# Performance work log

Hardware: AMD Instinct MI355X
Metric: run time of the kernel (lower is better)

Reference implementation:

```python
import jax, jax.numpy as jnp
import numpy as np

NUM_HEADS = 16
KERNEL_SIZE = 13


def setup_inputs() -> dict:
    key = jax.random.key(0)
    ks = jax.random.split(key, 6)
    B, L, C = 4, 4096, 512
    H, K = NUM_HEADS, KERNEL_SIZE
    x = jax.random.normal(ks[0], (B, L, C), dtype=jnp.float32)
    qkv_w = jax.random.normal(ks[1], (C, 3 * C), dtype=jnp.float32) * 0.02
    qkv_b = jnp.zeros((3 * C,), dtype=jnp.float32)
    rpb = jax.random.normal(ks[2], (H, 2 * K - 1), dtype=jnp.float32) * 0.02
    proj_w = jax.random.normal(ks[3], (C, C), dtype=jnp.float32) * 0.02
    proj_b = jnp.zeros((C,), dtype=jnp.float32)
    return {"x": x, "qkv_w": qkv_w, "qkv_b": qkv_b, "rpb": rpb,
            "proj_w": proj_w, "proj_b": proj_b}


def reference(x, qkv_w, qkv_b, rpb, proj_w, proj_b):
    B, L, C = x.shape
    H, K = NUM_HEADS, KERNEL_SIZE
    hd = C // H
    scale = hd ** -0.5
    kh = K // 2

    # qkv projection -> q,k,v each [B,H,L,hd]
    qkv = (x @ qkv_w + qkv_b).reshape(B, L, 3, H, hd).transpose(2, 0, 3, 1, 4)
    q, k, v = qkv[0] * scale, qkv[1], qkv[2]

    # NATTEN window: start index clamped so window stays in-bounds
    pos = jnp.arange(L)
    ni = jnp.clip(pos - kh, 0, L - K)              # [L] window start per query
    idx = ni[:, None] + jnp.arange(K)[None, :]     # [L,K] key positions
    # rpb index: (key_pos - query_pos) + (K-1)
    rpb_idx = (ni - pos + (K - 1))[:, None] + jnp.arange(K)[None, :]  # [L,K]

    k_win = k[:, :, idx, :]                        # [B,H,L,K,hd]
    v_win = v[:, :, idx, :]                        # [B,H,L,K,hd]

    attn = jnp.einsum('bhld,bhlkd->bhlk', q, k_win) + rpb[:, rpb_idx][None]
    attn = jax.nn.softmax(attn, axis=-1)

    out = jnp.einsum('bhlk,bhlkd->bhld', attn, v_win)  # [B,H,L,hd]
    out = out.transpose(0, 2, 1, 3).reshape(B, L, C)
    return out @ proj_w + proj_b
```

## Files before the change

kernel.cpp:

```cpp
#include <hip/hip_runtime.h>
#include <hip/hip_bf16.h>
#include <stdint.h>


typedef __attribute__((ext_vector_type(8))) short short8;
typedef __attribute__((ext_vector_type(4))) float f32x4;
typedef __attribute__((ext_vector_type(8))) unsigned short u16x8;
typedef __attribute__((ext_vector_type(4))) float float4v;

#define NB 4
#define NL 4096
#define NC 512
#define NH 16
#define HD 32
#define KW 13
#define KHALF 6
#define NM (NB*NL)

__device__ __forceinline__ float b2f(unsigned short u) {
  union { unsigned int i; float f; } x; x.i = ((unsigned int)u) << 16; return x.f;
}
__device__ __forceinline__ unsigned short f2b(float f) {
  __hip_bfloat16 h = __float2bfloat16(f);
  return __builtin_bit_cast(unsigned short, h);
}
__device__ __forceinline__ void gll16(const unsigned short* g, unsigned short* l) {
  __builtin_amdgcn_global_load_lds(
      (const __attribute__((address_space(1))) void*)g,
      (__attribute__((address_space(3))) void*)l, 16, 0, 0);
}

__global__ __launch_bounds__(256) void cvt_f32_bf16(const float* __restrict__ in,
                                                    unsigned short* __restrict__ out) {
  long i = (long)blockIdx.x * 256 + threadIdx.x;
  const float4v* in4 = (const float4v*)in;
  float4v a = in4[i * 2];
  float4v b = in4[i * 2 + 1];
  u16x8 u;
  u[0] = f2b(a.x); u[1] = f2b(a.y); u[2] = f2b(a.z); u[3] = f2b(a.w);
  u[4] = f2b(b.x); u[5] = f2b(b.y); u[6] = f2b(b.z); u[7] = f2b(b.w);
  ((u16x8*)out)[i] = u;
}

__global__ __launch_bounds__(256) void transpose_bf16(const float* __restrict__ in,
                                                      unsigned short* __restrict__ out,
                                                      int R, int C) {
  __shared__ float t[32][33];
  int c0 = blockIdx.x * 32;
  int r0 = blockIdx.y * 32;
  int tx = threadIdx.x;
  int ty = threadIdx.y;
  #pragma unroll
  for (int i = ty; i < 32; i += 8)
    t[i][tx] = in[(long)(r0 + i) * C + c0 + tx];
  __syncthreads();
  #pragma unroll
  for (int i = ty; i < 32; i += 8)
    out[(long)(c0 + i) * R + r0 + tx] = f2b(t[tx][i]);
}


__device__ __forceinline__ void stage_half(const unsigned short* __restrict__ G,
                                           long rowBase, int K, int kt,
                                           unsigned short* ldsDst, int tid) {
  int r  = tid >> 3;
  int ch = (tid & 7) ^ (r & 7);
  const unsigned short* s0 = G + (rowBase + r) * (long)K + kt * 64 + ch * 8;
  gll16(s0, ldsDst + tid * 8);
  gll16(s0 + 64 * (long)K, ldsDst + 4096 + tid * 8);
}

#define BAR() __builtin_amdgcn_s_barrier()
#define LGK0() asm volatile("s_waitcnt lgkmcnt(0)" ::: "memory")
#define VM(N) asm volatile("s_waitcnt vmcnt(" #N ")" ::: "memory")

#define DS_A(BUF, QM) do { \
  const char* _ba = (const char*)(lds + (BUF)*16384 + wm*8192); \
  _Pragma("unroll") for (int ii = 0; ii < 4; ++ii) { \
    int _row = ((QM)*4+ii)*16 + lr; \
    _Pragma("unroll") for (int kb = 0; kb < 2; ++kb) \
      af[ii][kb] = *(const short8*)(_ba + _row*128 + (((kb*4+lk) ^ lr7) * 16)); \
  } \
} while (0)

#define DS_B(BUF, QN, BF) do { \
  const char* _bb = (const char*)(lds + 32768 + (BUF)*16384 + (wn>>1)*8192); \
  _Pragma("unroll") for (int jj = 0; jj < 2; ++jj) { \
    int _row = (wn&1)*64 + ((QN)*2+jj)*16 + lr; \
    _Pragma("unroll") for (int kb = 0; kb < 2; ++kb) \
      BF[jj][kb] = *(const short8*)(_bb + _row*128 + (((kb*4+lk) ^ lr7) * 16)); \
  } \
} while (0)

#define MMA(QM, QN, BF) do { \
  __builtin_amdgcn_s_setprio(1); \
  _Pragma("unroll") for (int ii = 0; ii < 4; ++ii) \
    _Pragma("unroll") for (int jj = 0; jj < 2; ++jj) \
      _Pragma("unroll") for (int kb = 0; kb < 2; ++kb) \
        acc[(QM)*4+ii][(QN)*2+jj] = __builtin_amdgcn_mfma_f32_16x16x32_bf16( \
            af[ii][kb], BF[jj][kb], acc[(QM)*4+ii][(QN)*2+jj], 0, 0, 0); \
  __builtin_amdgcn_s_setprio(0); \
} while (0)

template<int OUT_BF16>
__global__ __launch_bounds__(512, 2)
void gemm256(const unsigned short* __restrict__ A,
             const unsigned short* __restrict__ BT,
             const float* __restrict__ bias,
             void* __restrict__ Cout,
             int M, int N, int K, int tilesN) {
  __shared__ __align__(16) unsigned short lds[65536];

  int tid = threadIdx.x;
  int nwg = gridDim.x;
  int cpx = nwg >> 3;
  int wg  = ((int)blockIdx.x & 7) * cpx + ((int)blockIdx.x >> 3);
  int tm = wg / tilesN, tn = wg % tilesN;
  long mBase = (long)tm * 256;
  long nBase = (long)tn * 256;

  int lane = tid & 63, wave = tid >> 6;
  int wm = wave >> 2;
  int wn = wave & 3;
  int lr = lane & 15, lk = lane >> 4, lr7 = lr & 7;

  unsigned short* A0h0 = lds;
  unsigned short* A0h1 = lds + 8192;
  unsigned short* A1h0 = lds + 16384;
  unsigned short* A1h1 = lds + 16384 + 8192;
  unsigned short* B0h0 = lds + 32768;
  unsigned short* B0h1 = lds + 32768 + 8192;
  unsigned short* B1h0 = lds + 32768 + 16384;
  unsigned short* B1h1 = lds + 32768 + 16384 + 8192;

  f32x4 acc[8][4];
  #pragma unroll
  for (int i = 0; i < 8; ++i)
    #pragma unroll
    for (int j = 0; j < 4; ++j) acc[i][j] = (f32x4){0.f, 0.f, 0.f, 0.f};

  short8 af[4][2], bf0[2][2], bf1[2][2];

  stage_half(BT, nBase,       K, 0, B0h0, tid);
  stage_half(BT, nBase + 128, K, 0, B0h1, tid);
  stage_half(A,  mBase,       K, 0, A0h0, tid);
  stage_half(A,  mBase + 128, K, 0, A0h1, tid);
  stage_half(BT, nBase,       K, 1, B1h0, tid);
  stage_half(BT, nBase + 128, K, 1, B1h1, tid);
  VM(4);
  BAR();

  #pragma unroll 1
  for (int it = 0; it < 4; ++it) {
    int kt = it * 2;
    bool s2 = (kt + 2) < 8;
    bool s3 = (kt + 3) < 8;

    DS_A(0, 0);
    DS_B(0, 0, bf0);
    stage_half(A, mBase, K, kt + 1, A1h0, tid);
    BAR(); LGK0();
    MMA(0, 0, bf0);
    BAR();
    DS_B(0, 1, bf1);
    stage_half(A, mBase + 128, K, kt + 1, A1h1, tid);
    BAR(); LGK0();
    MMA(0, 1, bf1);
    BAR();
    DS_A(0, 1);
    if (s2) stage_half(BT, nBase, K, kt + 2, B0h0, tid);
    BAR(); LGK0();
    MMA(1, 1, bf1);
    BAR();
    if (s2) { stage_half(BT, nBase + 128, K, kt + 2, B0h1, tid); VM(4); }
    else    { VM(0); }
    BAR();
    MMA(1, 0, bf0);
    BAR();
    DS_A(1, 0);
    DS_B(1, 0, bf0);
    if (s2) stage_half(A, mBase, K, kt + 2, A0h0, tid);
    BAR(); LGK0();
    MMA(0, 0, bf0);
    BAR();
    DS_B(1, 1, bf1);
    if (s2) stage_half(A, mBase + 128, K, kt + 2, A0h1, tid);
    BAR(); LGK0();
    MMA(0, 1, bf1);
    BAR();
    DS_A(1, 1);
    if (s3) stage_half(BT, nBase, K, kt + 3, B1h0, tid);
    BAR(); LGK0();
    MMA(1, 1, bf1);
    BAR();
    if (s3) { stage_half(BT, nBase + 128, K, kt + 3, B1h1, tid); VM(4); }
    BAR();
    MMA(1, 0, bf0);
    BAR();
  }

  long rowb = mBase + wm * 128 + (lane >> 4) * 4;
  int  colb = (int)nBase + wn * 64 + lr;
  if (OUT_BF16) {
    unsigned short* C = (unsigned short*)Cout;
    #pragma unroll
    for (int mi = 0; mi < 8; ++mi)
      #pragma unroll
      for (int nj = 0; nj < 4; ++nj) {
        int col = colb + nj * 16;
        float bv = bias[col];
        #pragma unroll
        for (int r = 0; r < 4; ++r)
          C[(rowb + mi * 16 + r) * (long)N + col] = f2b(acc[mi][nj][r] + bv);
      }
  } else {
    float* C = (float*)Cout;
    #pragma unroll
    for (int mi = 0; mi < 8; ++mi)
      #pragma unroll
      for (int nj = 0; nj < 4; ++nj) {
        int col = colb + nj * 16;
        float bv = bias[col];
        #pragma unroll
        for (int r = 0; r < 4; ++r)
          C[(rowb + mi * 16 + r) * (long)N + col] = acc[mi][nj][r] + bv;
      }
  }
}

__global__ __launch_bounds__(256)
void natt(const unsigned short* __restrict__ qkv, const float* __restrict__ rpb,
          unsigned short* __restrict__ out) {
  int tid = blockIdx.x * 256 + threadIdx.x;
  int h = tid & 15;
  int l = (tid >> 4) & (NL - 1);
  int b = tid >> 16;
  const float scale = 0.17677669529663687f;

  long qb = ((long)(b * NL + l) * 3) * NC + h * HD;
  float q[HD];
  {
    const u16x8* q8 = (const u16x8*)(qkv + qb);
    #pragma unroll
    for (int w = 0; w < 4; ++w) {
      u16x8 u = q8[w];
      #pragma unroll
      for (int e = 0; e < 8; ++e) q[w * 8 + e] = b2f(u[e]) * scale;
    }
  }

  int ni = l - KHALF;
  if (ni < 0) ni = 0;
  if (ni > NL - KW) ni = NL - KW;
  const float* rb = rpb + h * (2 * KW - 1) + (ni - l + KW - 1);

  float p[KW];
  float mx = -1e30f;
  #pragma unroll
  for (int j = 0; j < KW; ++j) {
    long kb = ((long)(b * NL + ni + j) * 3 + 1) * NC + h * HD;
    const u16x8* k8 = (const u16x8*)(qkv + kb);
    float s = 0.f;
    #pragma unroll
    for (int w = 0; w < 4; ++w) {
      u16x8 u = k8[w];
      #pragma unroll
      for (int e = 0; e < 8; ++e) s += q[w * 8 + e] * b2f(u[e]);
    }
    s += rb[j];
    p[j] = s;
    mx = fmaxf(mx, s);
  }

  float sum = 0.f;
  #pragma unroll
  for (int j = 0; j < KW; ++j) { p[j] = __expf(p[j] - mx); sum += p[j]; }
  float inv = 1.0f / sum;

  float o[HD];
  #pragma unroll
  for (int d = 0; d < HD; ++d) o[d] = 0.f;
  #pragma unroll
  for (int j = 0; j < KW; ++j) {
    long vb = ((long)(b * NL + ni + j) * 3 + 2) * NC + h * HD;
    const u16x8* v8 = (const u16x8*)(qkv + vb);
    float wj = p[j] * inv;
    #pragma unroll
    for (int w = 0; w < 4; ++w) {
      u16x8 u = v8[w];
      #pragma unroll
      for (int e = 0; e < 8; ++e) o[w * 8 + e] += wj * b2f(u[e]);
    }
  }

  unsigned short* op = out + (long)(b * NL + l) * NC + h * HD;
  #pragma unroll
  for (int w = 0; w < 4; ++w) {
    u16x8 u;
    #pragma unroll
    for (int e = 0; e < 8; ++e) u[e] = f2b(o[w * 8 + e]);
    *((u16x8*)(op + w * 8)) = u;
  }
}

extern "C" void kernel_launch(void* const* d_in, const int* in_sizes, int n_in,
                              void* d_out, int out_size, void* d_ws, size_t ws_size,
                              hipStream_t stream) {
  const float* x      = (const float*)d_in[0];
  const float* qkv_w  = (const float*)d_in[1];
  const float* qkv_b  = (const float*)d_in[2];
  const float* rpb    = (const float*)d_in[3];
  const float* proj_w = (const float*)d_in[4];
  const float* proj_b = (const float*)d_in[5];
  float* out = (float*)d_out;

  char* ws = (char*)d_ws;
  unsigned short* xb     = (unsigned short*)(ws);
  unsigned short* qkvwT  = (unsigned short*)(ws + 16777216);
  unsigned short* projwT = (unsigned short*)(ws + 18350080);
  unsigned short* qkvo   = (unsigned short*)(ws + 18874368);
  unsigned short* attno  = (unsigned short*)(ws + 69206016);

  cvt_f32_bf16<<<dim3(4096), dim3(256), 0, stream>>>(x, xb);
  transpose_bf16<<<dim3(48, 16), dim3(32, 8), 0, stream>>>(qkv_w, qkvwT, 512, 1536);
  transpose_bf16<<<dim3(16, 16), dim3(32, 8), 0, stream>>>(proj_w, projwT, 512, 512);
  gemm256<1><<<dim3(384), dim3(512), 0, stream>>>(xb, qkvwT, qkv_b, qkvo,
                                                  NM, 1536, 512, 6);
  natt<<<dim3(1024), dim3(256), 0, stream>>>(qkvo, rpb, attno);
  gemm256<0><<<dim3(128), dim3(512), 0, stream>>>(attno, projwT, proj_b, out,
                                                  NM, 512, 512, 2);
}
```

Baseline: 109.2 us.

## Shrink GEMM tile to 256x128 with 4x2 wave grid and merged pipeline phases

The GEMM tile drops from 256x256 to 256x128. The 8 waves are rearranged into a 4x2 grid, each computing 64x64. This doubles the workgroup count for both projections (768 and 256 blocks), so the small output GEMM fills more CUs. Each wave holds half the accumulators and less LDS, and several barrier-separated MMA phases are merged to cut synchronisation. The trade-off is lower arithmetic intensity per tile and more redundant A-tile loads across blocks.

```diff
diff --git a/kernel.cpp b/kernel.cpp
--- a/kernel.cpp
+++ b/kernel.cpp
@@ -75,18 +75,18 @@
 #define VM(N) asm volatile("s_waitcnt vmcnt(" #N ")" ::: "memory")
 
 #define DS_A(BUF, QM) do { \
-  const char* _ba = (const char*)(lds + (BUF)*16384 + wm*8192); \
-  _Pragma("unroll") for (int ii = 0; ii < 4; ++ii) { \
-    int _row = ((QM)*4+ii)*16 + lr; \
+  const char* _ba = (const char*)(lds + (BUF)*16384); \
+  _Pragma("unroll") for (int ii = 0; ii < 2; ++ii) { \
+    int _row = wm*64 + ((QM)*2+ii)*16 + lr; \
     _Pragma("unroll") for (int kb = 0; kb < 2; ++kb) \
       af[ii][kb] = *(const short8*)(_ba + _row*128 + (((kb*4+lk) ^ lr7) * 16)); \
   } \
 } while (0)
 
 #define DS_B(BUF, QN, BF) do { \
-  const char* _bb = (const char*)(lds + 32768 + (BUF)*16384 + (wn>>1)*8192); \
+  const char* _bb = (const char*)(lds + 32768 + (BUF)*8192); \
   _Pragma("unroll") for (int jj = 0; jj < 2; ++jj) { \
-    int _row = (wn&1)*64 + ((QN)*2+jj)*16 + lr; \
+    int _row = wn*64 + ((QN)*2+jj)*16 + lr; \
     _Pragma("unroll") for (int kb = 0; kb < 2; ++kb) \
       BF[jj][kb] = *(const short8*)(_bb + _row*128 + (((kb*4+lk) ^ lr7) * 16)); \
   } \
@@ -94,11 +94,11 @@
 
 #define MMA(QM, QN, BF) do { \
   __builtin_amdgcn_s_setprio(1); \
-  _Pragma("unroll") for (int ii = 0; ii < 4; ++ii) \
+  _Pragma("unroll") for (int ii = 0; ii < 2; ++ii) \
     _Pragma("unroll") for (int jj = 0; jj < 2; ++jj) \
       _Pragma("unroll") for (int kb = 0; kb < 2; ++kb) \
-        acc[(QM)*4+ii][(QN)*2+jj] = __builtin_amdgcn_mfma_f32_16x16x32_bf16( \
-            af[ii][kb], BF[jj][kb], acc[(QM)*4+ii][(QN)*2+jj], 0, 0, 0); \
+        acc[(QM)*2+ii][(QN)*2+jj] = __builtin_amdgcn_mfma_f32_16x16x32_bf16( \
+            af[ii][kb], BF[jj][kb], acc[(QM)*2+ii][(QN)*2+jj], 0, 0, 0); \
   __builtin_amdgcn_s_setprio(0); \
 } while (0)
 
@@ -109,7 +109,7 @@
              const float* __restrict__ bias,
              void* __restrict__ Cout,
              int M, int N, int K, int tilesN) {
-  __shared__ __align__(16) unsigned short lds[65536];
+  __shared__ __align__(16) unsigned short lds[49152];
 
   int tid = threadIdx.x;
   int nwg = gridDim.x;
@@ -117,37 +117,33 @@
   int wg  = ((int)blockIdx.x & 7) * cpx + ((int)blockIdx.x >> 3);
   int tm = wg / tilesN, tn = wg % tilesN;
   long mBase = (long)tm * 256;
-  long nBase = (long)tn * 256;
+  long nBase = (long)tn * 128;
 
   int lane = tid & 63, wave = tid >> 6;
-  int wm = wave >> 2;
-  int wn = wave & 3;
+  int wm = wave >> 1;
+  int wn = wave & 1;
   int lr = lane & 15, lk = lane >> 4, lr7 = lr & 7;
 
   unsigned short* A0h0 = lds;
   unsigned short* A0h1 = lds + 8192;
   unsigned short* A1h0 = lds + 16384;
   unsigned short* A1h1 = lds + 16384 + 8192;
-  unsigned short* B0h0 = lds + 32768;
-  unsigned short* B0h1 = lds + 32768 + 8192;
-  unsigned short* B1h0 = lds + 32768 + 16384;
-  unsigned short* B1h1 = lds + 32768 + 16384 + 8192;
-
-  f32x4 acc[8][4];
-  #pragma unroll
-  for (int i = 0; i < 8; ++i)
+  unsigned short* B0   = lds + 32768;
+  unsigned short* B1   = lds + 32768 + 8192;
+
+  f32x4 acc[4][4];
+  #pragma unroll
+  for (int i = 0; i < 4; ++i)
     #pragma unroll
     for (int j = 0; j < 4; ++j) acc[i][j] = (f32x4){0.f, 0.f, 0.f, 0.f};
 
-  short8 af[4][2], bf0[2][2], bf1[2][2];
-
-  stage_half(BT, nBase,       K, 0, B0h0, tid);
-  stage_half(BT, nBase + 128, K, 0, B0h1, tid);
+  short8 af[2][2], bf0[2][2], bf1[2][2];
+
+  stage_half(BT, nBase,       K, 0, B0,   tid);
   stage_half(A,  mBase,       K, 0, A0h0, tid);
   stage_half(A,  mBase + 128, K, 0, A0h1, tid);
-  stage_half(BT, nBase,       K, 1, B1h0, tid);
-  stage_half(BT, nBase + 128, K, 1, B1h1, tid);
-  VM(4);
+  stage_half(BT, nBase,       K, 1, B1,   tid);
+  VM(2);
   BAR();
 
   #pragma unroll 1
@@ -158,53 +154,46 @@
 
     DS_A(0, 0);
     DS_B(0, 0, bf0);
-    stage_half(A, mBase, K, kt + 1, A1h0, tid);
+    DS_B(0, 1, bf1);
+    stage_half(A, mBase,       K, kt + 1, A1h0, tid);
+    stage_half(A, mBase + 128, K, kt + 1, A1h1, tid);
     BAR(); LGK0();
     MMA(0, 0, bf0);
-    BAR();
-    DS_B(0, 1, bf1);
-    stage_half(A, mBase + 128, K, kt + 1, A1h1, tid);
-    BAR(); LGK0();
     MMA(0, 1, bf1);
     BAR();
     DS_A(0, 1);
-    if (s2) stage_half(BT, nBase, K, kt + 2, B0h0, tid);
+    if (s2) stage_half(BT, nBase, K, kt + 2, B0, tid);
     BAR(); LGK0();
     MMA(1, 1, bf1);
-    BAR();
-    if (s2) { stage_half(BT, nBase + 128, K, kt + 2, B0h1, tid); VM(4); }
-    else    { VM(0); }
-    BAR();
     MMA(1, 0, bf0);
+    if (s2) { VM(2); } else { VM(0); }
     BAR();
     DS_A(1, 0);
     DS_B(1, 0, bf0);
-    if (s2) stage_half(A, mBase, K, kt + 2, A0h0, tid);
+    DS_B(1, 1, bf1);
+    if (s2) {
+      stage_half(A, mBase,       K, kt + 2, A0h0, tid);
+      stage_half(A, mBase + 128, K, kt + 2, A0h1, tid);
+    }
     BAR(); LGK0();
     MMA(0, 0, bf0);
-    BAR();
-    DS_B(1, 1, bf1);
-    if (s2) stage_half(A, mBase + 128, K, kt + 2, A0h1, tid);
-    BAR(); LGK0();
     MMA(0, 1, bf1);
     BAR();
     DS_A(1, 1);
-    if (s3) stage_half(BT, nBase, K, kt + 3, B1h0, tid);
+    if (s3) stage_half(BT, nBase, K, kt + 3, B1, tid);
     BAR(); LGK0();
     MMA(1, 1, bf1);
+    MMA(1, 0, bf0);
+    if (s2) VM(2);
     BAR();
-    if (s3) { stage_half(BT, nBase + 128, K, kt + 3, B1h1, tid); VM(4); }
-    BAR();
-    MMA(1, 0, bf0);
-    BAR();
-  }
-
-  long rowb = mBase + wm * 128 + (lane >> 4) * 4;
+  }
+
+  long rowb = mBase + wm * 64 + (lane >> 4) * 4;
   int  colb = (int)nBase + wn * 64 + lr;
   if (OUT_BF16) {
     unsigned short* C = (unsigned short*)Cout;
     #pragma unroll
-    for (int mi = 0; mi < 8; ++mi)
+    for (int mi = 0; mi < 4; ++mi)
       #pragma unroll
       for (int nj = 0; nj < 4; ++nj) {
         int col = colb + nj * 16;
@@ -216,7 +205,7 @@
   } else {
     float* C = (float*)Cout;
     #pragma unroll
-    for (int mi = 0; mi < 8; ++mi)
+    for (int mi = 0; mi < 4; ++mi)
       #pragma unroll
       for (int nj = 0; nj < 4; ++nj) {
         int col = colb + nj * 16;
@@ -324,9 +313,9 @@
   cvt_f32_bf16<<<dim3(4096), dim3(256), 0, stream>>>(x, xb);
   transpose_bf16<<<dim3(48, 16), dim3(32, 8), 0, stream>>>(qkv_w, qkvwT, 512, 1536);
   transpose_bf16<<<dim3(16, 16), dim3(32, 8), 0, stream>>>(proj_w, projwT, 512, 512);
-  gemm256<1><<<dim3(384), dim3(512), 0, stream>>>(xb, qkvwT, qkv_b, qkvo,
-                                                  NM, 1536, 512, 6);
+  gemm256<1><<<dim3(768), dim3(512), 0, stream>>>(xb, qkvwT, qkv_b, qkvo,
+                                                  NM, 1536, 512, 12);
   natt<<<dim3(1024), dim3(256), 0, stream>>>(qkvo, rpb, attno);
-  gemm256<0><<<dim3(128), dim3(512), 0, stream>>>(attno, projwT, proj_b, out,
-                                                  NM, 512, 512, 2);
-}
+  gemm256<0><<<dim3(256), dim3(512), 0, stream>>>(attno, projwT, proj_b, out,
+                                                  NM, 512, 512, 4);
+}
```

Result: no change. 108.8 us (-0.4%).
